# Performance work log

Hardware: AMD Instinct MI355X
Metric: run time of the kernel (lower is better)

Reference implementation:

```python
import jax, jax.numpy as jnp
import numpy as np


def _build_transform():
    # Deterministic re-creation of SegmentationAugmentation.build_3d_transform
    # with flip=True, offset=0.1, scale=0.2, rotate=True.
    rng = np.random.default_rng(0)
    t = np.eye(4, dtype=np.float32)
    for i in range(3):
        if rng.random() > 0.5:
            t[i, i] *= -1.0
        t[i, 3] = 0.1 * (rng.random() * 2.0 - 1.0)
        t[i, i] *= 1.0 + 0.2 * (rng.random() * 2.0 - 1.0)
    a = rng.random() * 2.0 * np.pi
    s, c = np.sin(a), np.cos(a)
    rot = np.array([[c, -s, 0, 0], [s, c, 0, 0], [0, 0, 1, 0], [0, 0, 0, 1]],
                   dtype=np.float32)
    return t @ rot


def _affine_grid(theta, size):
    # theta: [B,3,4]; size: (B,C,D,H,W); align_corners=False.
    B, C, D, H, W = size
    def lin(n):
        # pixel-center normalized coords: (2i+1)/n - 1
        return (2.0 * jnp.arange(n, dtype=jnp.float32) + 1.0) / n - 1.0
    z, y, x = jnp.meshgrid(lin(D), lin(H), lin(W), indexing='ij')
    pts = jnp.stack([x, y, z], axis=-1)  # [D,H,W,3], (x,y,z) order as in torch
    return (jnp.einsum('bij,dhwj->bdhwi', theta[:, :, :3], pts)
            + theta[:, None, None, None, :, 3])


def _grid_sample_3d_border(inp, grid):
    # trilinear grid_sample, padding_mode='border', align_corners=False.
    # inp: [B,C,D,H,W]; grid: [B,Do,Ho,Wo,3] with (x,y,z) normalized coords.
    B, C, D, H, W = inp.shape
    Do, Ho, Wo = grid.shape[1:4]

    def unnorm(cn, n):
        # align_corners=False unnormalize, then border clamp
        return jnp.clip(((cn + 1.0) * n - 1.0) * 0.5, 0.0, n - 1.0)

    x = unnorm(grid[..., 0], W)
    y = unnorm(grid[..., 1], H)
    z = unnorm(grid[..., 2], D)
    x0 = jnp.floor(x); y0 = jnp.floor(y); z0 = jnp.floor(z)
    fx, fy, fz = x - x0, y - y0, z - z0
    x0i = x0.astype(jnp.int32); y0i = y0.astype(jnp.int32); z0i = z0.astype(jnp.int32)
    x1i = jnp.minimum(x0i + 1, W - 1)
    y1i = jnp.minimum(y0i + 1, H - 1)
    z1i = jnp.minimum(z0i + 1, D - 1)

    inp_flat = inp.reshape(B, C, D * H * W)
    N = Do * Ho * Wo
    out = jnp.zeros((B, C, N), dtype=inp.dtype)
    for zi, wz in ((z0i, 1.0 - fz), (z1i, fz)):
        for yi, wy in ((y0i, 1.0 - fy), (y1i, fy)):
            for xi, wx in ((x0i, 1.0 - fx), (x1i, fx)):
                idx = ((zi * H + yi) * W + xi).reshape(B, 1, N)
                v = jnp.take_along_axis(
                    inp_flat, jnp.broadcast_to(idx, (B, C, N)), axis=2)
                w = (wz * wy * wx).reshape(B, 1, N)
                out = out + v * w
    return out.reshape(B, C, Do, Ho, Wo)


def setup_inputs() -> dict:
    key = jax.random.key(0)
    k1, k2 = jax.random.split(key)
    input_g = jax.random.normal(k1, (8, 1, 128, 128, 128), dtype=jnp.float32)
    label_g = jax.random.uniform(k2, (8, 1, 128, 128, 128), dtype=jnp.float32)
    transform = jnp.asarray(_build_transform())
    return {"input_g": input_g, "label_g": label_g, "transform": transform}


def reference(input_g, label_g, transform):
    # transpose(-3,-1): swap depth and width axes
    inp = jnp.swapaxes(input_g, -3, -1)
    lab = jnp.swapaxes(label_g, -3, -1)
    B = inp.shape[0]
    theta = jnp.broadcast_to(transform[:3][None], (B, 3, 4)).astype(jnp.float32)
    grid = _affine_grid(theta, inp.shape)
    aug_inp = _grid_sample_3d_border(inp, grid)
    aug_lab = _grid_sample_3d_border(lab, grid)
    aug_inp = jnp.swapaxes(aug_inp, -3, -1)
    aug_lab = jnp.swapaxes(aug_lab, -3, -1)
    return aug_inp, aug_lab > 0.5
```

## Files before the change

### kernel.cpp

```cpp
#include <hip/hip_runtime.h>


#define NV 128
#define TOTAL (8 * NV * NV * NV)

__global__ __launch_bounds__(128) void seg_aug_kernel(
    const float* __restrict__ in,
    const float* __restrict__ lab,
    const float* __restrict__ T,
    float* __restrict__ out_in,
    float* __restrict__ out_lab)
{
#pragma clang fp contract(off)
    __shared__ float s[8 * NV];

    const int t  = threadIdx.x;
    const int o3 = blockIdx.x & (NV - 1);
    const int o2 = (blockIdx.x >> 7) & (NV - 1);
    const int b  = blockIdx.x >> 14;

    float p2 = (2.0f * (float)o2 + 1.0f) / 128.0f - 1.0f;
    float p3 = (2.0f * (float)o3 + 1.0f) / 128.0f - 1.0f;
    float ux = (T[0] * p2 + T[1] * p3) + T[3];
    float uy = (T[4] * p2 + T[5] * p3) + T[7];
    float gx = ((ux + 1.0f) * 128.0f - 1.0f) * 0.5f;
    float gy = ((uy + 1.0f) * 128.0f - 1.0f) * 0.5f;
    gx = fminf(fmaxf(gx, 0.0f), 127.0f);
    gy = fminf(fmaxf(gy, 0.0f), 127.0f);
    float fx0f = floorf(gx), fy0f = floorf(gy);
    float fx = gx - fx0f;
    float fy = gy - fy0f;
    const int ix0 = __builtin_amdgcn_readfirstlane((int)fx0f);
    const int iy0 = __builtin_amdgcn_readfirstlane((int)fy0f);
    const int ix1 = min(ix0 + 1, NV - 1);
    const int iy1 = min(iy0 + 1, NV - 1);
    float wx0 = 1.0f - fx, wx1 = fx;
    float wy0 = 1.0f - fy, wy1 = fy;

    const size_t bbase = (size_t)b << 21;
    const float* ibp = in  + bbase;
    const float* lbp = lab + bbase;
    {
        const int rid = t >> 5;
        const int seg = t & 31;
        const int ixS = (rid & 2) ? ix1 : ix0;
        const int iyS = (rid & 1) ? iy1 : iy0;
        const int off = (ixS * NV + iyS) * NV + seg * 4;
        __builtin_amdgcn_global_load_lds(ibp + off, &s[t * 4],       16, 0, 0);
        __builtin_amdgcn_global_load_lds(lbp + off, &s[512 + t * 4], 16, 0, 0);
    }

    float p4 = (2.0f * (float)t + 1.0f) / 128.0f - 1.0f;
    float uz = T[10] * p4 + T[11];
    float gz = ((uz + 1.0f) * 128.0f - 1.0f) * 0.5f;
    gz = fminf(fmaxf(gz, 0.0f), 127.0f);
    float fz0f = floorf(gz);
    float fz = gz - fz0f;
    int iz0 = (int)fz0f;
    float wz0 = 1.0f - fz, wz1 = fz;

    const int zb = min(iz0, NV - 2);
    const bool hi = (iz0 == NV - 1);

    __syncthreads();

    #define PAIR(ROW, A, B) \
        float A = s[(ROW) * NV + zb]; \
        float B = s[(ROW) * NV + zb + 1];

    PAIR(0, ia00, ib00)
    PAIR(1, ia01, ib01)
    PAIR(2, ia10, ib10)
    PAIR(3, ia11, ib11)
    PAIR(4, la00, lb00)
    PAIR(5, la01, lb01)
    PAIR(6, la10, lb10)
    PAIR(7, la11, lb11)
    #undef PAIR

    float vi000 = hi ? ib00 : ia00;
    float vi010 = hi ? ib01 : ia01;
    float vi100 = hi ? ib10 : ia10;
    float vi110 = hi ? ib11 : ia11;
    float vl000 = hi ? lb00 : la00;
    float vl010 = hi ? lb01 : la01;
    float vl100 = hi ? lb10 : la10;
    float vl110 = hi ? lb11 : la11;

    float tz0y0 = wz0 * wy0, tz0y1 = wz0 * wy1;
    float tz1y0 = wz1 * wy0, tz1y1 = wz1 * wy1;
    float w1 = tz0y0 * wx0, w2 = tz0y0 * wx1;
    float w3 = tz0y1 * wx0, w4 = tz0y1 * wx1;
    float w5 = tz1y0 * wx0, w6 = tz1y0 * wx1;
    float w7 = tz1y1 * wx0, w8 = tz1y1 * wx1;

    float acc_i = 0.0f;
    acc_i = acc_i + vi000 * w1;
    acc_i = acc_i + vi100 * w2;
    acc_i = acc_i + vi010 * w3;
    acc_i = acc_i + vi110 * w4;
    acc_i = acc_i + ib00 * w5;
    acc_i = acc_i + ib10 * w6;
    acc_i = acc_i + ib01 * w7;
    acc_i = acc_i + ib11 * w8;

    float acc_l = 0.0f;
    acc_l = acc_l + vl000 * w1;
    acc_l = acc_l + vl100 * w2;
    acc_l = acc_l + vl010 * w3;
    acc_l = acc_l + vl110 * w4;
    acc_l = acc_l + lb00 * w5;
    acc_l = acc_l + lb10 * w6;
    acc_l = acc_l + lb01 * w7;
    acc_l = acc_l + lb11 * w8;

    const int oidx = blockIdx.x * NV + t;
    out_in[oidx]  = acc_i;
    out_lab[oidx] = (acc_l > 0.5f) ? 1.0f : 0.0f;
}

extern "C" void kernel_launch(void* const* d_in, const int* in_sizes, int n_in,
                              void* d_out, int out_size, void* d_ws, size_t ws_size,
                              hipStream_t stream) {
    const float* in  = (const float*)d_in[0];
    const float* lab = (const float*)d_in[1];
    const float* T   = (const float*)d_in[2];
    float* out_in  = (float*)d_out;
    float* out_lab = (float*)d_out + TOTAL;

    dim3 grid(TOTAL / 128);
    dim3 block(128);
    seg_aug_kernel<<<grid, block, 0, stream>>>(in, lab, T, out_in, out_lab);
}
```

Baseline: 245.1 us.

## Interleave input and label in LDS and compute both with packed float2 math

Replaces the direct global-to-LDS loads with register float4 loads that are written to shared memory interleaved as (input, label) pairs. Each thread then reads 8 float2 values from LDS instead of 16 scalars and accumulates both outputs with 2-wide vector arithmetic, which may map to packed FMA/mul instructions. A zero-padded tail removes the edge-case select logic for iz0 == 127, since the weight on the out-of-range sample is zero. In exchange the data now passes through VGPRs before reaching LDS, and the writes to LDS are explicit.

```diff
diff --git a/kernel.cpp b/kernel.cpp
--- a/kernel.cpp
+++ b/kernel.cpp
@@ -3,6 +3,8 @@
 
 #define NV 128
 #define TOTAL (8 * NV * NV * NV)
+
+typedef float v2f __attribute__((ext_vector_type(2)));
 
 __global__ __launch_bounds__(128) void seg_aug_kernel(
     const float* __restrict__ in,
@@ -12,7 +14,7 @@
     float* __restrict__ out_lab)
 {
 #pragma clang fp contract(off)
-    __shared__ float s[8 * NV];
+    __shared__ __align__(16) float s[4 * NV * 2 + 2];
 
     const int t  = threadIdx.x;
     const int o3 = blockIdx.x & (NV - 1);
@@ -38,17 +40,13 @@
     float wy0 = 1.0f - fy, wy1 = fy;
 
     const size_t bbase = (size_t)b << 21;
-    const float* ibp = in  + bbase;
-    const float* lbp = lab + bbase;
-    {
-        const int rid = t >> 5;
-        const int seg = t & 31;
-        const int ixS = (rid & 2) ? ix1 : ix0;
-        const int iyS = (rid & 1) ? iy1 : iy0;
-        const int off = (ixS * NV + iyS) * NV + seg * 4;
-        __builtin_amdgcn_global_load_lds(ibp + off, &s[t * 4],       16, 0, 0);
-        __builtin_amdgcn_global_load_lds(lbp + off, &s[512 + t * 4], 16, 0, 0);
-    }
+    const int rid = t >> 5;
+    const int seg = t & 31;
+    const int ixS = (rid & 2) ? ix1 : ix0;
+    const int iyS = (rid & 1) ? iy1 : iy0;
+    const int goff = (ixS * NV + iyS) * NV + seg * 4;
+    const float4 i4 = *(const float4*)(in  + bbase + goff);
+    const float4 l4 = *(const float4*)(lab + bbase + goff);
 
     float p4 = (2.0f * (float)t + 1.0f) / 128.0f - 1.0f;
     float uz = T[10] * p4 + T[11];
@@ -56,36 +54,23 @@
     gz = fminf(fmaxf(gz, 0.0f), 127.0f);
     float fz0f = floorf(gz);
     float fz = gz - fz0f;
-    int iz0 = (int)fz0f;
+    const int iz0 = (int)fz0f;
     float wz0 = 1.0f - fz, wz1 = fz;
 
-    const int zb = min(iz0, NV - 2);
-    const bool hi = (iz0 == NV - 1);
+    if (t < 2) s[4 * NV * 2 + t] = 0.0f;
 
+    {
+        float* d = &s[(rid * NV + seg * 4) * 2];
+        ((float4*)d)[0] = make_float4(i4.x, l4.x, i4.y, l4.y);
+        ((float4*)d)[1] = make_float4(i4.z, l4.z, i4.w, l4.w);
+    }
     __syncthreads();
 
-    #define PAIR(ROW, A, B) \
-        float A = s[(ROW) * NV + zb]; \
-        float B = s[(ROW) * NV + zb + 1];
-
-    PAIR(0, ia00, ib00)
-    PAIR(1, ia01, ib01)
-    PAIR(2, ia10, ib10)
-    PAIR(3, ia11, ib11)
-    PAIR(4, la00, lb00)
-    PAIR(5, la01, lb01)
-    PAIR(6, la10, lb10)
-    PAIR(7, la11, lb11)
-    #undef PAIR
-
-    float vi000 = hi ? ib00 : ia00;
-    float vi010 = hi ? ib01 : ia01;
-    float vi100 = hi ? ib10 : ia10;
-    float vi110 = hi ? ib11 : ia11;
-    float vl000 = hi ? lb00 : la00;
-    float vl010 = hi ? lb01 : la01;
-    float vl100 = hi ? lb10 : la10;
-    float vl110 = hi ? lb11 : la11;
+    const v2f* srow = (const v2f*)s;
+    v2f a0 = srow[0 * NV + iz0], b0 = srow[0 * NV + iz0 + 1];
+    v2f a1 = srow[1 * NV + iz0], b1 = srow[1 * NV + iz0 + 1];
+    v2f a2 = srow[2 * NV + iz0], b2 = srow[2 * NV + iz0 + 1];
+    v2f a3 = srow[3 * NV + iz0], b3 = srow[3 * NV + iz0 + 1];
 
     float tz0y0 = wz0 * wy0, tz0y1 = wz0 * wy1;
     float tz1y0 = wz1 * wy0, tz1y1 = wz1 * wy1;
@@ -94,29 +79,19 @@
     float w5 = tz1y0 * wx0, w6 = tz1y0 * wx1;
     float w7 = tz1y1 * wx0, w8 = tz1y1 * wx1;
 
-    float acc_i = 0.0f;
-    acc_i = acc_i + vi000 * w1;
-    acc_i = acc_i + vi100 * w2;
-    acc_i = acc_i + vi010 * w3;
-    acc_i = acc_i + vi110 * w4;
-    acc_i = acc_i + ib00 * w5;
-    acc_i = acc_i + ib10 * w6;
-    acc_i = acc_i + ib01 * w7;
-    acc_i = acc_i + ib11 * w8;
-
-    float acc_l = 0.0f;
-    acc_l = acc_l + vl000 * w1;
-    acc_l = acc_l + vl100 * w2;
-    acc_l = acc_l + vl010 * w3;
-    acc_l = acc_l + vl110 * w4;
-    acc_l = acc_l + lb00 * w5;
-    acc_l = acc_l + lb10 * w6;
-    acc_l = acc_l + lb01 * w7;
-    acc_l = acc_l + lb11 * w8;
+    v2f acc = {0.0f, 0.0f};
+    acc = acc + a0 * w1;
+    acc = acc + a2 * w2;
+    acc = acc + a1 * w3;
+    acc = acc + a3 * w4;
+    acc = acc + b0 * w5;
+    acc = acc + b2 * w6;
+    acc = acc + b1 * w7;
+    acc = acc + b3 * w8;
 
     const int oidx = blockIdx.x * NV + t;
-    out_in[oidx]  = acc_i;
-    out_lab[oidx] = (acc_l > 0.5f) ? 1.0f : 0.0f;
+    out_in[oidx]  = acc.x;
+    out_lab[oidx] = (acc.y > 0.5f) ? 1.0f : 0.0f;
 }
 
 extern "C" void kernel_launch(void* const* d_in, const int* in_sizes, int n_in,
```

Result: no change. 246.1 us (+0.4%).
